# Kernel optimization log

Hardware: AMD Instinct MI355X
Metric: run time of the kernel (lower is better)

Reference implementation:

```python
import jax, jax.numpy as jnp
import numpy as np

B, N, K, NUM_CLASSES = 8, 4096, 20, 40


def _knn_idx(x, k):
    # x: [B, N, D] -> indices of k nearest neighbors (self excluded), [B, N, k]
    sq = jnp.sum(x * x, axis=-1)  # [B, N]
    dist = sq[:, :, None] + sq[:, None, :] - 2.0 * jnp.einsum('bnd,bmd->bnm', x, x)
    dist = jnp.where(jnp.eye(x.shape[1], dtype=bool)[None], jnp.inf, dist)
    return jax.lax.top_k(-dist, k)[1]


def _edge_conv(x, idx, params):
    # PyG EdgeConv with max aggregation: max_j MLP([x_i, x_j - x_i])
    x_j = jax.vmap(lambda xb, ib: xb[ib])(x, idx)              # [B, N, K, D]
    x_i = jnp.broadcast_to(x[:, :, None, :], x_j.shape)        # [B, N, K, D]
    h = jnp.concatenate([x_i, x_j - x_i], axis=-1)             # [B, N, K, 2D]
    for w, b in params:
        h = jax.nn.relu(h @ w + b)
    return jnp.max(h, axis=2)                                  # [B, N, out]


def setup_inputs() -> dict:
    key = jax.random.key(0)
    ks = jax.random.split(key, 12)

    def lin(k, i, o):  # torch Linear default init
        k1, k2 = jax.random.split(k)
        s = 1.0 / np.sqrt(i)
        return (jax.random.uniform(k1, (i, o), jnp.float32, -s, s),
                jax.random.uniform(k2, (o,), jnp.float32, -s, s))

    inp = {
        'pos': jax.random.normal(ks[0], (B * N, 3), jnp.float32),
        'batch': jnp.repeat(jnp.arange(B, dtype=jnp.int32), N),
    }
    names = [('m1w1', 'm1b1', 6, 64), ('m1w2', 'm1b2', 64, 64), ('m1w3', 'm1b3', 64, 64),
             ('m2w1', 'm2b1', 128, 128), ('m2w2', 'm2b2', 128, 128), ('m2w3', 'm2b3', 128, 256),
             ('lin0_w', 'lin0_b', 256, 512), ('lin1_w', 'lin1_b', 512, 256),
             ('lin2_w', 'lin2_b', 256, 256), ('lin3_w', 'lin3_b', 256, NUM_CLASSES)]
    for t, (wn, bn, i, o) in enumerate(names):
        w, b = lin(ks[t + 1], i, o)
        inp[wn] = w
        inp[bn] = b
    return inp


def reference(pos, batch, m1w1, m1b1, m1w2, m1b2, m1w3, m1b3,
              m2w1, m2b1, m2w2, m2b2, m2w3, m2b3,
              lin0_w, lin0_b, lin1_w, lin1_b, lin2_w, lin2_b, lin3_w, lin3_b):
    x = pos.reshape(B, N, 3)
    x = _edge_conv(x, _knn_idx(x, K), [(m1w1, m1b1), (m1w2, m1b2), (m1w3, m1b3)])   # [B,N,64]
    x = _edge_conv(x, _knn_idx(x, K), [(m2w1, m2b1), (m2w2, m2b2), (m2w3, m2b3)])   # [B,N,256]
    x = jax.nn.relu(x @ lin0_w + lin0_b)                                            # [B,N,512]
    x = jax.ops.segment_max(x.reshape(B * N, -1), batch, num_segments=B)            # [B,512]
    x = jax.nn.relu(x @ lin1_w + lin1_b)
    x = jax.nn.relu(x @ lin2_w + lin2_b)   # dropout is identity in eval mode
    x = x @ lin3_w + lin3_b
    return jax.nn.log_softmax(x, axis=-1)
```

## Files before the change

### kernel.cpp

```cpp
#include <hip/hip_runtime.h>

#define DEVI static __device__ __forceinline__

typedef __attribute__((ext_vector_type(4))) float f32x4;
typedef __attribute__((ext_vector_type(8))) short short8;
typedef __attribute__((ext_vector_type(4))) short short4v;
typedef __attribute__((ext_vector_type(8))) __bf16 bf16x8;

#define N_    4096
#define KNN_  20
#define NPTS  32768

DEVI unsigned short f2bf(float f){
  unsigned u = __float_as_uint(f);
  u += 0x7FFFu + ((u >> 16) & 1u);
  return (unsigned short)(u >> 16);
}
DEVI float bf2f(unsigned short s){ return __uint_as_float(((unsigned)s) << 16); }
DEVI float bf2fs(short s){ return __uint_as_float(((unsigned)(unsigned short)s) << 16); }
DEVI unsigned umin32(unsigned a, unsigned b){ return a < b ? a : b; }
DEVI unsigned umax32(unsigned a, unsigned b){ return a > b ? a : b; }

DEVI f32x4 mfma16(short8 a, short8 b, f32x4 c){
  return __builtin_amdgcn_mfma_f32_16x16x32_bf16(
      __builtin_bit_cast(bf16x8, a), __builtin_bit_cast(bf16x8, b), c, 0, 0, 0);
}

DEVI short8 lds_frag(const unsigned short* buf, int row, int k0, int strideS, int swzMask){
  return *(const short8*)(buf + row*strideS + (k0 ^ ((row & swzMask) << 3)));
}
DEVI void lds_put8(unsigned short* buf, int row, int k0, int strideS, int swzMask, short8 v){
  *(short8*)(buf + row*strideS + (k0 ^ ((row & swzMask) << 3))) = v;
}

DEVI void ins32(unsigned K, unsigned (&a)[20]){
#pragma unroll
  for (int t = 19; t >= 1; --t) a[t] = umin32(a[t], umax32(a[t-1], K));
  a[0] = umin32(a[0], K);
}
DEVI void ins64(double K, double (&a)[20]){
#pragma unroll
  for (int t = 19; t >= 1; --t) a[t] = fmin(a[t], fmax(a[t-1], K));
  a[0] = fmin(a[0], K);
}

DEVI void stage_body(const float* __restrict__ src, unsigned short* __restrict__ dh,
                     unsigned short* __restrict__ dl, int K, int Nw, int KT, int lblk){
  int tid = lblk*256 + (int)threadIdx.x;
  int l = tid & 63;
  int kk = (tid >> 6) % KT;
  int nt = tid / (64*KT);
  int n = nt*16 + (l & 15);
  int kb = kk*32 + ((l >> 4) << 3);
#pragma unroll
  for (int e=0;e<8;++e){
    int k = kb + e;
    float w = (k < K) ? src[(size_t)k*Nw + n] : 0.f;
    unsigned short h = f2bf(w);
    dh[(size_t)tid*8 + e] = h;
    if (dl) dl[(size_t)tid*8 + e] = f2bf(w - bf2f(h));
  }
}

__global__ __launch_bounds__(256) void stage_all_k(const float* __restrict__ pos,
    unsigned short* __restrict__ p3h, unsigned short* __restrict__ p3l, float* __restrict__ nrm3,
    const float* __restrict__ m1w1, const float* __restrict__ m1w2, const float* __restrict__ m1w3,
    const float* __restrict__ m2w1, const float* __restrict__ m2w2, const float* __restrict__ m2w3,
    const float* __restrict__ l0w,
    unsigned short* __restrict__ W1h, unsigned short* __restrict__ W1l,
    unsigned short* __restrict__ W2h, unsigned short* __restrict__ W2l,
    unsigned short* __restrict__ W3h, unsigned short* __restrict__ W3l,
    unsigned short* __restrict__ V1, unsigned short* __restrict__ V2, unsigned short* __restrict__ V3,
    unsigned short* __restrict__ W0){
  const int blk = blockIdx.x;
  if (blk < 128){
    int p = blk*256 + (int)threadIdx.x;
    float x = pos[(size_t)p*3], y = pos[(size_t)p*3+1], z = pos[(size_t)p*3+2];
    float v[8] = {x, y, z, 0.f, 0.f, 0.f, 0.f, 0.f};
#pragma unroll
    for (int c = 0; c < 8; ++c){
      unsigned short h = f2bf(v[c]);
      p3h[(size_t)p*8 + c] = h;
      p3l[(size_t)p*8 + c] = f2bf(v[c] - bf2f(h));
    }
    nrm3[p] = fmaf(x, x, fmaf(y, y, z*z));
    return;
  }
  int b = blk - 128;
  if      (b < 1)  stage_body(m1w1, W1h, W1l, 6,   64,  1, b);
  else if (b < 3)  stage_body(m1w2, W2h, W2l, 64,  64,  2, b-1);
  else if (b < 5)  stage_body(m1w3, W3h, W3l, 64,  64,  2, b-3);
  else if (b < 13) stage_body(m2w1, V1, nullptr, 128, 128, 4, b-5);
  else if (b < 21) stage_body(m2w2, V2, nullptr, 128, 128, 4, b-13);
  else if (b < 37) stage_body(m2w3, V3, nullptr, 128, 256, 4, b-21);
  else             stage_body(l0w,  W0, nullptr, 256, 512, 8, b-37);
}

template<int MODE>
__global__ __launch_bounds__(256) void knn_k(const unsigned short* __restrict__ Xh,
                                             const unsigned short* __restrict__ Xl,
                                             const float* __restrict__ nrm,
                                             unsigned* __restrict__ pk){
  constexpr int BSTR = MODE ? 4096 : 512;
  constexpr int OBL  = MODE ? 16384 : 2048;
  constexpr int OBUF = MODE ? 32768 : 4096;
  constexpr int OTHR = OBUF + 6144;
  constexpr int OSQ  = OTHR + 256;
  constexpr int SM   = MODE ? (OSQ + 512) : 15360;
  __shared__ __align__(16) char smem[SM];
  unsigned short* BhA = (unsigned short*)(smem);
  unsigned short* BlA = (unsigned short*)(smem + OBL);
  unsigned* buf      = (unsigned*)(smem + OBUF);
  unsigned* rowThr   = (unsigned*)(smem + OTHR);
  float* sqjA        = (float*)(smem + OSQ);
  unsigned* mD       = (unsigned*)(smem);

  const int blk = blockIdx.x;
  const int rt = blk & 63, ch = (blk >> 6) & 1, bb = blk >> 7;
  const int rowbase = rt * 64, cbase = ch * 2048;
  const size_t gb = (size_t)bb * N_;
  const int tid = threadIdx.x, lane = tid & 63, wid = tid >> 6;
  const int l15 = lane & 15, g = lane >> 4, kL = g << 3, r0 = g << 2;
  const int qidx = wid*16 + l15;

  if (tid < 64) rowThr[tid] = 0xFFFFFFFFu;

  short8 qh0 = {0,0,0,0,0,0,0,0}, qh1 = {0,0,0,0,0,0,0,0};
  short8 ql0 = {0,0,0,0,0,0,0,0}, ql1 = {0,0,0,0,0,0,0,0};
  if (MODE == 1){
    const size_t ab = (gb + rowbase + qidx) * 64;
    qh0 = *(const short8*)(Xh + ab + kL);
    qh1 = *(const short8*)(Xh + ab + 32 + kL);
    ql0 = *(const short8*)(Xl + ab + kL);
    ql1 = *(const short8*)(Xl + ab + 32 + kL);
  } else {
    if (g == 0){
      const size_t ab = (gb + rowbase + qidx) * 8;
      qh0 = *(const short8*)(Xh + ab);
      ql0 = *(const short8*)(Xl + ab);
    }
  }
  const float si = nrm[gb + rowbase + qidx];

  unsigned arr[20];
#pragma unroll
  for (int t = 0; t < 20; ++t) arr[t] = 0xFFFFFFFFu;
  int cnt = 0;
  bool selfR[4];
#pragma unroll
  for (int r = 0; r < 4; ++r) selfR[r] = (l15 == r0 + r);

  if (MODE == 1){
    for (int f = tid; f < 512; f += 256){
      int lf = f & 63, half = (f >> 6) & 1, ct = f >> 7;
      int row = ct*16 + (lf & 15);
      int col = half*32 + ((lf >> 4) << 3);
      const size_t src = (gb + cbase + row) * 64 + col;
      *(short8*)(BhA + f*8) = *(const short8*)(Xh + src);
      *(short8*)(BlA + f*8) = *(const short8*)(Xl + src);
    }
  } else {
    if (tid < 64)       *(short8*)(BhA + tid*8)      = *(const short8*)(Xh + (gb + cbase + tid)*8);
    else if (tid < 128) *(short8*)(BlA + (tid-64)*8) = *(const short8*)(Xl + (gb + cbase + (tid-64))*8);
  }
  if (tid < 64) sqjA[tid] = nrm[gb + cbase + tid];
  __syncthreads();

  for (int c = 0; c < 32; ++c){
    const int cur = c & 1;
    const unsigned short* Bh = BhA + cur*BSTR;
    const unsigned short* Bl = BlA + cur*BSTR;
    const float* sqj = sqjA + cur*64;
    const bool selfTile = (cbase + c*64 == rowbase);
    const bool more = (c + 1 < 32);

    short8 nh0 = {0,0,0,0,0,0,0,0}, nh1 = {0,0,0,0,0,0,0,0};
    short8 nl0 = {0,0,0,0,0,0,0,0}, nl1 = {0,0,0,0,0,0,0,0};
    float nsq = 0.f;
    if (more){
      if (MODE == 1){
#pragma unroll
        for (int ff = 0; ff < 2; ++ff){
          int f = tid + ff*256;
          int lf = f & 63, half = (f >> 6) & 1, ct = f >> 7;
          int row = ct*16 + (lf & 15);
          int col = half*32 + ((lf >> 4) << 3);
          const size_t src = (gb + cbase + (c+1)*64 + row) * 64 + col;
          if (ff == 0){ nh0 = *(const short8*)(Xh + src); nl0 = *(const short8*)(Xl + src); }
          else        { nh1 = *(const short8*)(Xh + src); nl1 = *(const short8*)(Xl + src); }
        }
      } else {
        if (tid < 64)       nh0 = *(const short8*)(Xh + (gb + cbase + (c+1)*64 + tid)*8);
        else if (tid < 128) nl0 = *(const short8*)(Xl + (gb + cbase + (c+1)*64 + (tid-64))*8);
      }
      if (tid < 64) nsq = nrm[gb + cbase + (c+1)*64 + tid];
    }

    unsigned kb16[16];
#pragma unroll
    for (int ct = 0; ct < 4; ++ct){
      f32x4 acc = {0.f,0.f,0.f,0.f};
      if (MODE == 1){
        const int fb = lane*8;
        short8 ch0 = *(const short8*)(Bh + (ct*2+0)*512 + fb);
        short8 ch1 = *(const short8*)(Bh + (ct*2+1)*512 + fb);
        short8 cl0 = *(const short8*)(Bl + (ct*2+0)*512 + fb);
        short8 cl1 = *(const short8*)(Bl + (ct*2+1)*512 + fb);
        acc = mfma16(ch0, qh0, acc); acc = mfma16(ch1, qh1, acc);
        acc = mfma16(cl0, qh0, acc); acc = mfma16(cl1, qh1, acc);
        acc = mfma16(ch0, ql0, acc); acc = mfma16(ch1, ql1, acc);
      } else {
        short8 cb = {0,0,0,0,0,0,0,0}, cl_ = {0,0,0,0,0,0,0,0};
        if (g == 0){
          cb  = *(const short8*)(Bh + (ct*16 + l15)*8);
          cl_ = *(const short8*)(Bl + (ct*16 + l15)*8);
        }
        acc = mfma16(cb,  qh0, acc);
        acc = mfma16(cl_, qh0, acc);
        acc = mfma16(cb,  ql0, acc);
      }
      f32x4 sj4 = *(const f32x4*)(sqj + ct*16 + r0);
#pragma unroll
      for (int r = 0; r < 4; ++r){
        float dv = fmaxf(fmaf(-2.f, acc[r], si + sj4[r]), 0.f);
        kb16[ct*4 + r] = __float_as_uint(dv);
      }
    }

    {
      unsigned thrUp = rowThr[qidx] | 0x7FFu;
#pragma unroll
      for (int i = 0; i < 16; ++i){
        unsigned b = kb16[i];
        if (b <= thrUp){
          if (selfTile && (i >> 2) == wid && selfR[i & 3]) continue;
          unsigned kb = (b & ~0x7FFu) | (unsigned)(c*64 + (i >> 2)*16 + r0 + (i & 3));
          if (cnt < 6){ buf[cnt*256 + tid] = kb; ++cnt; }
          else ins32(kb, arr);
        }
      }
      for (int t = 0; t < cnt; ++t) ins32(buf[t*256 + tid], arr);
      cnt = 0;
      atomicMin(&rowThr[qidx], arr[19]);
    }

    if (more){
      unsigned short* BhN = BhA + (cur^1)*BSTR;
      unsigned short* BlN = BlA + (cur^1)*BSTR;
      if (MODE == 1){
        *(short8*)(BhN + tid*8)       = nh0;
        *(short8*)(BhN + (tid+256)*8) = nh1;
        *(short8*)(BlN + tid*8)       = nl0;
        *(short8*)(BlN + (tid+256)*8) = nl1;
      } else {
        if (tid < 64)       *(short8*)(BhN + tid*8)      = nh0;
        else if (tid < 128) *(short8*)(BlN + (tid-64)*8) = nl0;
      }
      if (tid < 64) sqjA[(cur^1)*64 + tid] = nsq;
    }
    __syncthreads();
  }
  __syncthreads();
  if (g > 0){
#pragma unroll
    for (int t = 0; t < 20; ++t) mD[(qidx*3 + g-1)*20 + t] = arr[t];
  }
  __syncthreads();
  if (g == 0){
    for (int gg = 0; gg < 3; ++gg)
#pragma unroll
      for (int t = 0; t < 20; ++t) ins32(mD[(qidx*3 + gg)*20 + t], arr);
    const size_t gp = gb + rowbase + qidx;
#pragma unroll
    for (int t = 0; t < 20; ++t) pk[((size_t)(ch*20 + t))*NPTS + gp] = arr[t];
  }
}

__global__ __launch_bounds__(256) void knn_merge_k(const unsigned* __restrict__ pk,
                                                   int* __restrict__ idx){
  const int p = blockIdx.x*256 + threadIdx.x;
  double arr[20];
#pragma unroll
  for (int t = 0; t < 20; ++t){
    unsigned k = pk[(size_t)t*NPTS + p];
    unsigned long long K = (((unsigned long long)(k & ~0x7FFu)) << 1) | (k & 0x7FFu);
    arr[t] = __builtin_bit_cast(double, K);
  }
#pragma unroll
  for (int t = 0; t < 20; ++t){
    unsigned k = pk[(size_t)(20 + t)*NPTS + p];
    unsigned long long K = (((unsigned long long)(k & ~0x7FFu)) << 1) | (2048u + (k & 0x7FFu));
    ins64(__builtin_bit_cast(double, K), arr);
  }
  int* o = idx + (size_t)p*KNN_;
#pragma unroll
  for (int t = 0; t < 20; ++t)
    o[t] = (int)(__builtin_bit_cast(unsigned long long, arr[t]) & 0xFFFu);
}

__global__ __launch_bounds__(256) void ec1_k(const float* __restrict__ pos, const int* __restrict__ idx1,
    const unsigned short* __restrict__ W1h, const unsigned short* __restrict__ W1l,
    const unsigned short* __restrict__ W2h, const unsigned short* __restrict__ W2l,
    const unsigned short* __restrict__ W3h, const unsigned short* __restrict__ W3l,
    const float* __restrict__ b1, const float* __restrict__ b2, const float* __restrict__ b3,
    unsigned short* __restrict__ x1h, unsigned short* __restrict__ x1l, float* __restrict__ nrm1){
  __shared__ __align__(16) char smem[51200];
  unsigned short* Ah  = (unsigned short*)(smem);
  unsigned short* Al  = (unsigned short*)(smem + 5120);
  unsigned short* H1h = (unsigned short*)(smem + 10240);
  unsigned short* H1l = (unsigned short*)(smem + 20480);
  unsigned short* H2h = (unsigned short*)(smem + 30720);
  unsigned short* H2l = (unsigned short*)(smem + 40960);
  float* dump = (float*)(smem);
  const int p0 = blockIdx.x * 4;
  const int bb = p0 >> 12;
  const int tid = threadIdx.x, lane = tid & 63, wid = tid >> 6;
  const int l15 = lane & 15, g = lane >> 4, r0 = g << 2;

  if (tid < 80){
    int p = p0 + tid/20, slot = tid%20;
    int j = idx1[(size_t)p*KNN_ + slot];
    int gj = (bb << 12) + j;
    float a6[6];
    a6[0] = pos[(size_t)p*3]; a6[1] = pos[(size_t)p*3+1]; a6[2] = pos[(size_t)p*3+2];
    a6[3] = pos[(size_t)gj*3]   - a6[0];
    a6[4] = pos[(size_t)gj*3+1] - a6[1];
    a6[5] = pos[(size_t)gj*3+2] - a6[2];
    int mt = tid >> 4, lrow = tid & 15;
    short8 vh, vl, zz = {0,0,0,0,0,0,0,0};
#pragma unroll
    for (int c=0;c<8;++c){
      float v = (c < 6) ? a6[c] : 0.f;
      unsigned short h = f2bf(v);
      vh[c] = (short)h;
      vl[c] = (short)f2bf(v - bf2f(h));
    }
    *(short8*)(Ah + (mt*64 + lrow)*8) = vh;
    *(short8*)(Al + (mt*64 + lrow)*8) = vl;
#pragma unroll
    for (int gg=1;gg<4;++gg){
      *(short8*)(Ah + (mt*64 + gg*16 + lrow)*8) = zz;
      *(short8*)(Al + (mt*64 + gg*16 + lrow)*8) = zz;
    }
  }
  __syncthreads();
  const int nt = wid;
  const int kk2 = nt >> 1, sub2 = (nt & 1)*2 + (g >> 1), e0 = (g & 1)*4;
  {
    short8 wh = *(const short8*)(W1h + ((size_t)nt*64 + lane)*8);
    short8 wl = *(const short8*)(W1l + ((size_t)nt*64 + lane)*8);
    f32x4 b4 = *(const f32x4*)(b1 + nt*16 + r0);
    for (int mt=0; mt<5; ++mt){
      short8 ah = *(const short8*)(Ah + (mt*64 + lane)*8);
      short8 al = *(const short8*)(Al + (mt*64 + lane)*8);
      f32x4 acc = {0.f,0.f,0.f,0.f};
      acc = mfma16(wh, ah, acc);
      acc = mfma16(wl, ah, acc);
      acc = mfma16(wh, al, acc);
      short4v vh4, vl4;
#pragma unroll
      for (int r=0;r<4;++r){
        float v = fmaxf(acc[r] + b4[r], 0.f);
        unsigned short h = f2bf(v);
        vh4[r] = (short)h;
        vl4[r] = (short)f2bf(v - bf2f(h));
      }
      *(short4v*)(H1h + ((mt*2 + kk2)*64 + sub2*16 + l15)*8 + e0) = vh4;
      *(short4v*)(H1l + ((mt*2 + kk2)*64 + sub2*16 + l15)*8 + e0) = vl4;
    }
  }
  __syncthreads();
  {
    short8 wh0 = *(const short8*)(W2h + ((size_t)(nt*2+0)*64 + lane)*8);
    short8 wh1 = *(const short8*)(W2h + ((size_t)(nt*2+1)*64 + lane)*8);
    short8 wl0 = *(const short8*)(W2l + ((size_t)(nt*2+0)*64 + lane)*8);
    short8 wl1 = *(const short8*)(W2l + ((size_t)(nt*2+1)*64 + lane)*8);
    f32x4 b4 = *(const f32x4*)(b2 + nt*16 + r0);
    for (int mt=0; mt<5; ++mt){
      short8 ah0 = *(const short8*)(H1h + ((mt*2+0)*64 + lane)*8);
      short8 ah1 = *(const short8*)(H1h + ((mt*2+1)*64 + lane)*8);
      short8 al0 = *(const short8*)(H1l + ((mt*2+0)*64 + lane)*8);
      short8 al1 = *(const short8*)(H1l + ((mt*2+1)*64 + lane)*8);
      f32x4 acc = {0.f,0.f,0.f,0.f};
      acc = mfma16(wh0, ah0, acc); acc = mfma16(wh1, ah1, acc);
      acc = mfma16(wl0, ah0, acc); acc = mfma16(wl1, ah1, acc);
      acc = mfma16(wh0, al0, acc); acc = mfma16(wh1, al1, acc);
      short4v vh4, vl4;
#pragma unroll
      for (int r=0;r<4;++r){
        float v = fmaxf(acc[r] + b4[r], 0.f);
        unsigned short h = f2bf(v);
        vh4[r] = (short)h;
        vl4[r] = (short)f2bf(v - bf2f(h));
      }
      *(short4v*)(H2h + ((mt*2 + kk2)*64 + sub2*16 + l15)*8 + e0) = vh4;
      *(short4v*)(H2l + ((mt*2 + kk2)*64 + sub2*16 + l15)*8 + e0) = vl4;
    }
  }
  __syncthreads();
  {
    short8 wh0 = *(const short8*)(W3h + ((size_t)(nt*2+0)*64 + lane)*8);
    short8 wh1 = *(const short8*)(W3h + ((size_t)(nt*2+1)*64 + lane)*8);
    short8 wl0 = *(const short8*)(W3l + ((size_t)(nt*2+0)*64 + lane)*8);
    short8 wl1 = *(const short8*)(W3l + ((size_t)(nt*2+1)*64 + lane)*8);
    f32x4 b4 = *(const f32x4*)(b3 + nt*16 + r0);
    for (int mt=0; mt<5; ++mt){
      short8 ah0 = *(const short8*)(H2h + ((mt*2+0)*64 + lane)*8);
      short8 ah1 = *(const short8*)(H2h + ((mt*2+1)*64 + lane)*8);
      short8 al0 = *(const short8*)(H2l + ((mt*2+0)*64 + lane)*8);
      short8 al1 = *(const short8*)(H2l + ((mt*2+1)*64 + lane)*8);
      f32x4 acc = {0.f,0.f,0.f,0.f};
      acc = mfma16(wh0, ah0, acc); acc = mfma16(wh1, ah1, acc);
      acc = mfma16(wl0, ah0, acc); acc = mfma16(wl1, ah1, acc);
      acc = mfma16(wh0, al0, acc); acc = mfma16(wh1, al1, acc);
      f32x4 o;
#pragma unroll
      for (int r=0;r<4;++r) o[r] = fmaxf(acc[r] + b4[r], 0.f);
      int edge = mt*16 + l15;
      *(f32x4*)(dump + edge*68 + nt*16 + r0) = o;
    }
  }
  __syncthreads();
  if (tid < 64){
    int p = tid >> 4, c4 = tid & 15;
    int st = tid % 20;
    float mx[4] = {0.f,0.f,0.f,0.f};
    for (int e=0;e<20;++e){
      int ee = st + e; if (ee >= 20) ee -= 20;
      f32x4 v = *(const f32x4*)(dump + (p*20 + ee)*68 + c4*4);
#pragma unroll
      for (int r=0;r<4;++r) mx[r] = fmaxf(mx[r], v[r]);
    }
    int gp = p0 + p;
    short4v h4, l4;
    float s = 0.f;
#pragma unroll
    for (int r=0;r<4;++r){
      float m = mx[r];
      unsigned short h = f2bf(m);
      h4[r] = (short)h;
      l4[r] = (short)f2bf(m - bf2f(h));
      s = fmaf(m, m, s);
    }
    *(short4v*)(x1h + (size_t)gp*64 + c4*4) = h4;
    *(short4v*)(x1l + (size_t)gp*64 + c4*4) = l4;
    s += __shfl_xor(s, 1); s += __shfl_xor(s, 2); s += __shfl_xor(s, 4); s += __shfl_xor(s, 8);
    if (c4 == 0) nrm1[gp] = s;
  }
}

__global__ __launch_bounds__(256) void ec2_k(const unsigned short* __restrict__ x1h, const int* __restrict__ idx2,
    const unsigned short* __restrict__ V1, const unsigned short* __restrict__ V2, const unsigned short* __restrict__ V3,
    const float* __restrict__ b1, const float* __restrict__ b2, const float* __restrict__ b3,
    unsigned short* __restrict__ x2b){
  __shared__ __align__(16) char smem[81920];
  unsigned short* A  = (unsigned short*)(smem);
  unsigned short* H1 = (unsigned short*)(smem + 40960);
  const int p0 = blockIdx.x * 8, bb = p0 >> 12;
  const int tid = threadIdx.x, lane = tid & 63, wid = tid >> 6;
  const int l15 = lane & 15, r0 = (lane >> 4) << 2;

  if (tid < 160){
    int p = p0 + tid/20, slot = tid%20;
    int j = idx2[(size_t)p*KNN_ + slot];
    int gj = (bb << 12) + j;
    const unsigned short* xi = x1h + (size_t)p*64;
    const unsigned short* xj = x1h + (size_t)gj*64;
    int mt = tid >> 4, lrow = tid & 15;
#pragma unroll
    for (int q=0;q<8;++q){
      short8 vi = *(const short8*)(xi + q*8);
      short8 vj = *(const short8*)(xj + q*8);
      short8 vd;
#pragma unroll
      for (int c=0;c<8;++c) vd[c] = (short)f2bf(bf2fs(vj[c]) - bf2fs(vi[c]));
      *(short8*)(A + (((mt*4 + (q>>2))*64) + (q&3)*16 + lrow)*8) = vi;
      *(short8*)(A + (((mt*4 + 2 + (q>>2))*64) + (q&3)*16 + lrow)*8) = vd;
    }
  }
  __syncthreads();

  {
    short8 w[2][4];
#pragma unroll
    for (int ni=0;ni<2;++ni)
#pragma unroll
      for (int kk=0;kk<4;++kk)
        w[ni][kk] = *(const short8*)(V1 + ((size_t)((wid*2+ni)*4+kk)*64 + lane)*8);
    f32x4 b4[2];
    b4[0] = *(const f32x4*)(b1 + (wid*2+0)*16 + r0);
    b4[1] = *(const f32x4*)(b1 + (wid*2+1)*16 + r0);
    for (int mt=0; mt<10; ++mt){
      short8 bfr[4];
#pragma unroll
      for (int kk=0;kk<4;++kk) bfr[kk] = *(const short8*)(A + ((mt*4+kk)*64 + lane)*8);
#pragma unroll
      for (int ni=0;ni<2;++ni){
        int nt = wid*2 + ni;
        f32x4 acc = {0.f,0.f,0.f,0.f};
#pragma unroll
        for (int kk=0;kk<4;++kk) acc = mfma16(w[ni][kk], bfr[kk], acc);
        short4v v4;
#pragma unroll
        for (int r=0;r<4;++r) v4[r] = (short)f2bf(fmaxf(acc[r] + b4[ni][r], 0.f));
        int kk2 = nt >> 1, sub2 = (nt & 1)*2 + (r0 >> 3);
        *(short4v*)(H1 + ((mt*4+kk2)*64 + sub2*16 + l15)*8 + (r0 & 4)) = v4;
      }
    }
  }
  __syncthreads();
  {
    short8 w[2][4];
#pragma unroll
    for (int ni=0;ni<2;++ni)
#pragma unroll
      for (int kk=0;kk<4;++kk)
        w[ni][kk] = *(const short8*)(V2 + ((size_t)((wid*2+ni)*4+kk)*64 + lane)*8);
    f32x4 b4[2];
    b4[0] = *(const f32x4*)(b2 + (wid*2+0)*16 + r0);
    b4[1] = *(const f32x4*)(b2 + (wid*2+1)*16 + r0);
    for (int mt=0; mt<10; ++mt){
      short8 bfr[4];
#pragma unroll
      for (int kk=0;kk<4;++kk) bfr[kk] = *(const short8*)(H1 + ((mt*4+kk)*64 + lane)*8);
#pragma unroll
      for (int ni=0;ni<2;++ni){
        int nt = wid*2 + ni;
        f32x4 acc = {0.f,0.f,0.f,0.f};
#pragma unroll
        for (int kk=0;kk<4;++kk) acc = mfma16(w[ni][kk], bfr[kk], acc);
        short4v v4;
#pragma unroll
        for (int r=0;r<4;++r) v4[r] = (short)f2bf(fmaxf(acc[r] + b4[ni][r], 0.f));
        int kk2 = nt >> 1, sub2 = (nt & 1)*2 + (r0 >> 3);
        *(short4v*)(A + ((mt*4+kk2)*64 + sub2*16 + l15)*8 + (r0 & 4)) = v4;
      }
    }
  }
  __syncthreads();
  for (int g2=0; g2<2; ++g2){
    {
      short8 w[2][4];
#pragma unroll
      for (int ni=0;ni<2;++ni)
#pragma unroll
        for (int kk=0;kk<4;++kk)
          w[ni][kk] = *(const short8*)(V3 + ((size_t)((g2*8 + wid*2+ni)*4+kk)*64 + lane)*8);
      f32x4 b4[2];
      b4[0] = *(const f32x4*)(b3 + (g2*8 + wid*2+0)*16 + r0);
      b4[1] = *(const f32x4*)(b3 + (g2*8 + wid*2+1)*16 + r0);
      for (int mt=0; mt<10; ++mt){
        short8 bfr[4];
#pragma unroll
        for (int kk=0;kk<4;++kk) bfr[kk] = *(const short8*)(A + ((mt*4+kk)*64 + lane)*8);
#pragma unroll
        for (int ni=0;ni<2;++ni){
          int ntl = wid*2 + ni;
          f32x4 acc = {0.f,0.f,0.f,0.f};
#pragma unroll
          for (int kk=0;kk<4;++kk) acc = mfma16(w[ni][kk], bfr[kk], acc);
          short4v v4;
#pragma unroll
          for (int r=0;r<4;++r) v4[r] = (short)f2bf(fmaxf(acc[r] + b4[ni][r], 0.f));
          int kk2 = ntl >> 1, sub2 = (ntl & 1)*2 + (r0 >> 3);
          *(short4v*)(H1 + ((mt*4+kk2)*64 + sub2*16 + l15)*8 + (r0 & 4)) = v4;
        }
      }
    }
    __syncthreads();
    if (tid < 128){
      int p = tid >> 4, c8 = tid & 15;
      int kk = c8 >> 2, sub = c8 & 3;
      unsigned short mx[8];
#pragma unroll
      for (int e=0;e<8;++e) mx[e] = 0;
      for (int e=0;e<20;++e){
        int ee = e + p + c8; ee -= (ee >= 20) ? 20 : 0; ee -= (ee >= 20) ? 20 : 0;
        int row = p*20 + ee;
        short8 v = *(const short8*)(H1 + (((row>>4)*4 + kk)*64 + sub*16 + (row & 15))*8);
#pragma unroll
        for (int k2=0;k2<8;++k2){
          unsigned short u = (unsigned short)v[k2];
          mx[k2] = u > mx[k2] ? u : mx[k2];
        }
      }
      short8 o;
#pragma unroll
      for (int k2=0;k2<8;++k2) o[k2] = (short)mx[k2];
      *(short8*)(x2b + (size_t)(p0 + p)*256 + g2*128 + c8*8) = o;
    }
    __syncthreads();
  }
}

__global__ __launch_bounds__(256) void lin0_k(const unsigned short* __restrict__ x2b, const unsigned short* __restrict__ W0s,
                                              const float* __restrict__ b0, unsigned* __restrict__ pool){
  __shared__ __align__(16) char smem[67584];
  unsigned short* A = (unsigned short*)(smem);
  unsigned* ploc = (unsigned*)(smem + 65536);
  const int blk = blockIdx.x; const size_t row0 = (size_t)blk * 128; const int bb = blk >> 5;
  const int tid = threadIdx.x, lane = tid & 63, wid = tid >> 6;
  for (int it = tid; it < 4096; it += 256){
    int row = it >> 5, q = (it & 31) << 3;
    lds_put8(A, row, q, 256, 7, *(const short8*)(x2b + (row0 + row)*256 + q));
  }
  ploc[tid] = 0u; ploc[tid+256] = 0u;
  __syncthreads();
  const int l15 = lane & 15, kL = (lane >> 4) << 3;
  short8 af[2][8];
#pragma unroll
  for (int m=0;m<2;++m)
#pragma unroll
    for (int kk=0;kk<8;++kk)
      af[m][kk] = lds_frag(A, (wid*2+m)*16 + l15, kk*32 + kL, 256, 7);
  for (int nt=0; nt<32; ++nt){
    f32x4 a0 = {0.f,0.f,0.f,0.f}, a1 = {0.f,0.f,0.f,0.f};
#pragma unroll
    for (int kk=0;kk<8;++kk){
      short8 w = *(const short8*)(W0s + ((size_t)(nt*8+kk)*64 + lane)*8);
      a0 = mfma16(af[0][kk], w, a0);
      a1 = mfma16(af[1][kk], w, a1);
    }
    int col = nt*16 + l15;
    float m = fmaxf(fmaxf(fmaxf(a0[0],a0[1]),fmaxf(a0[2],a0[3])),
                    fmaxf(fmaxf(a1[0],a1[1]),fmaxf(a1[2],a1[3])));
    m = fmaxf(m + b0[col], 0.f);
    atomicMax(&ploc[col], __float_as_uint(m));
  }
  __syncthreads();
  atomicMax(&pool[(size_t)bb*512 + tid], ploc[tid]);
  atomicMax(&pool[(size_t)bb*512 + tid + 256], ploc[tid+256]);
}

__global__ __launch_bounds__(256) void head8_k(const unsigned* __restrict__ pool,
    const float* __restrict__ w1, const float* __restrict__ bb1,
    const float* __restrict__ w2, const float* __restrict__ bb2,
    const float* __restrict__ w3, const float* __restrict__ bb3,
    float* __restrict__ out){
  __shared__ float pl[512];
  __shared__ float y1[256];
  __shared__ float y2[256];
  __shared__ float lg[40];
  const int row = blockIdx.x;
  const int tid = threadIdx.x;
  for (int it = tid; it < 512; it += 256) pl[it] = __uint_as_float(pool[row*512 + it]);
  __syncthreads();
  {
    float acc = bb1[tid];
    for (int k=0;k<512;++k) acc = fmaf(pl[k], w1[(size_t)k*256 + tid], acc);
    y1[tid] = fmaxf(acc, 0.f);
  }
  __syncthreads();
  {
    float acc = bb2[tid];
    for (int k=0;k<256;++k) acc = fmaf(y1[k], w2[(size_t)k*256 + tid], acc);
    y2[tid] = fmaxf(acc, 0.f);
  }
  __syncthreads();
  if (tid < 40){
    float acc = bb3[tid];
    for (int k=0;k<256;++k) acc = fmaf(y2[k], w3[(size_t)k*40 + tid], acc);
    lg[tid] = acc;
  }
  __syncthreads();
  if (tid < 40){
    float m = -__builtin_inff();
    for (int c2=0;c2<40;++c2) m = fmaxf(m, lg[c2]);
    float s = 0.f;
    for (int c2=0;c2<40;++c2) s += expf(lg[c2] - m);
    out[row*40 + tid] = lg[tid] - m - logf(s);
  }
}

extern "C" void kernel_launch(void* const* d_in, const int* in_sizes, int n_in,
                              void* d_out, int out_size, void* d_ws, size_t ws_size,
                              hipStream_t stream){
  (void)in_sizes; (void)n_in; (void)out_size; (void)ws_size;
  const float* pos  = (const float*)d_in[0];
  const float* m1w1 = (const float*)d_in[2];  const float* m1b1 = (const float*)d_in[3];
  const float* m1w2 = (const float*)d_in[4];  const float* m1b2 = (const float*)d_in[5];
  const float* m1w3 = (const float*)d_in[6];  const float* m1b3 = (const float*)d_in[7];
  const float* m2w1 = (const float*)d_in[8];  const float* m2b1 = (const float*)d_in[9];
  const float* m2w2 = (const float*)d_in[10]; const float* m2b2 = (const float*)d_in[11];
  const float* m2w3 = (const float*)d_in[12]; const float* m2b3 = (const float*)d_in[13];
  const float* l0w  = (const float*)d_in[14]; const float* l0b  = (const float*)d_in[15];
  const float* l1w  = (const float*)d_in[16]; const float* l1b  = (const float*)d_in[17];
  const float* l2w  = (const float*)d_in[18]; const float* l2b  = (const float*)d_in[19];
  const float* l3w  = (const float*)d_in[20]; const float* l3b  = (const float*)d_in[21];

  char* ws = (char*)d_ws;
  size_t o = 0;
  auto alloc = [&](size_t bytes){ size_t r = o; o += (bytes + 255) & ~(size_t)255; return r; };
  size_t o_idx1 = alloc((size_t)NPTS*20*4);
  size_t o_idx2 = alloc((size_t)NPTS*20*4);
  size_t o_x1h  = alloc((size_t)NPTS*64*2);
  size_t o_x1l  = alloc((size_t)NPTS*64*2);
  size_t o_nrm  = alloc((size_t)NPTS*4);
  size_t o_x2b  = alloc((size_t)NPTS*256*2);
  size_t o_pool = alloc(8*512*4);
  size_t o_p3h  = alloc((size_t)NPTS*8*2);
  size_t o_p3l  = alloc((size_t)NPTS*8*2);
  size_t o_nrm3 = alloc((size_t)NPTS*4);
  size_t o_pk   = alloc((size_t)2*20*NPTS*4);
  size_t o_W1h = alloc(4*1*64*8*2),  o_W1l = alloc(4*1*64*8*2);
  size_t o_W2h = alloc(4*2*64*8*2),  o_W2l = alloc(4*2*64*8*2);
  size_t o_W3h = alloc(4*2*64*8*2),  o_W3l = alloc(4*2*64*8*2);
  size_t o_V1  = alloc(8*4*64*8*2);
  size_t o_V2  = alloc(8*4*64*8*2);
  size_t o_V3  = alloc(16*4*64*8*2);
  size_t o_W0  = alloc(32*8*64*8*2);

  hipMemsetAsync(ws + o_pool, 0, 8*512*4, stream);

  stage_all_k<<<229,256,0,stream>>>(pos,
      (unsigned short*)(ws+o_p3h), (unsigned short*)(ws+o_p3l), (float*)(ws+o_nrm3),
      m1w1, m1w2, m1w3, m2w1, m2w2, m2w3, l0w,
      (unsigned short*)(ws+o_W1h), (unsigned short*)(ws+o_W1l),
      (unsigned short*)(ws+o_W2h), (unsigned short*)(ws+o_W2l),
      (unsigned short*)(ws+o_W3h), (unsigned short*)(ws+o_W3l),
      (unsigned short*)(ws+o_V1), (unsigned short*)(ws+o_V2), (unsigned short*)(ws+o_V3),
      (unsigned short*)(ws+o_W0));

  knn_k<0><<<1024,256,0,stream>>>((const unsigned short*)(ws+o_p3h), (const unsigned short*)(ws+o_p3l),
                                  (const float*)(ws+o_nrm3), (unsigned*)(ws+o_pk));
  knn_merge_k<<<128,256,0,stream>>>((const unsigned*)(ws+o_pk), (int*)(ws+o_idx1));

  ec1_k<<<8192,256,0,stream>>>(pos, (const int*)(ws+o_idx1),
      (const unsigned short*)(ws+o_W1h), (const unsigned short*)(ws+o_W1l),
      (const unsigned short*)(ws+o_W2h), (const unsigned short*)(ws+o_W2l),
      (const unsigned short*)(ws+o_W3h), (const unsigned short*)(ws+o_W3l),
      m1b1, m1b2, m1b3,
      (unsigned short*)(ws+o_x1h), (unsigned short*)(ws+o_x1l), (float*)(ws+o_nrm));

  knn_k<1><<<1024,256,0,stream>>>((const unsigned short*)(ws+o_x1h), (const unsigned short*)(ws+o_x1l),
                                  (const float*)(ws+o_nrm), (unsigned*)(ws+o_pk));
  knn_merge_k<<<128,256,0,stream>>>((const unsigned*)(ws+o_pk), (int*)(ws+o_idx2));

  ec2_k<<<4096,256,0,stream>>>((const unsigned short*)(ws+o_x1h), (const int*)(ws+o_idx2),
      (const unsigned short*)(ws+o_V1), (const unsigned short*)(ws+o_V2), (const unsigned short*)(ws+o_V3),
      m2b1, m2b2, m2b3, (unsigned short*)(ws+o_x2b));

  lin0_k<<<256,256,0,stream>>>((const unsigned short*)(ws+o_x2b), (const unsigned short*)(ws+o_W0),
                               l0b, (unsigned*)(ws+o_pool));

  head8_k<<<8,256,0,stream>>>((const unsigned*)(ws+o_pool), l1w, l1b, l2w, l2b, l3w, l3b, (float*)d_out);
}
```

Before: 575.8 us.

## Enlarge kNN blocks to 128 query rows with 512 threads sharing candidate tiles

The kNN kernel now runs 512 threads per block covering 128 query rows instead of 64, so each staged candidate tile in shared memory serves twice as many queries. This halves the global loads of candidate tiles, and each thread now loads one short8 per tile instead of two. Self-exclusion moves out of the inner selection loop into a single masked write before the loop. The cost is larger shared memory per block, half as many blocks, and possibly lower occupancy or load balance.

```diff
diff --git a/kernel.cpp b/kernel.cpp
--- a/kernel.cpp
+++ b/kernel.cpp
@@ -97,16 +97,16 @@
 }
 
 template<int MODE>
-__global__ __launch_bounds__(256) void knn_k(const unsigned short* __restrict__ Xh,
+__global__ __launch_bounds__(512) void knn_k(const unsigned short* __restrict__ Xh,
                                              const unsigned short* __restrict__ Xl,
                                              const float* __restrict__ nrm,
                                              unsigned* __restrict__ pk){
   constexpr int BSTR = MODE ? 4096 : 512;
   constexpr int OBL  = MODE ? 16384 : 2048;
   constexpr int OBUF = MODE ? 32768 : 4096;
-  constexpr int OTHR = OBUF + 6144;
-  constexpr int OSQ  = OTHR + 256;
-  constexpr int SM   = MODE ? (OSQ + 512) : 15360;
+  constexpr int OTHR = OBUF + 12288;
+  constexpr int OSQ  = OTHR + 512;
+  constexpr int SM   = MODE ? (OSQ + 512) : 30720;
   __shared__ __align__(16) char smem[SM];
   unsigned short* BhA = (unsigned short*)(smem);
   unsigned short* BlA = (unsigned short*)(smem + OBL);
@@ -116,14 +116,14 @@
   unsigned* mD       = (unsigned*)(smem);
 
   const int blk = blockIdx.x;
-  const int rt = blk & 63, ch = (blk >> 6) & 1, bb = blk >> 7;
-  const int rowbase = rt * 64, cbase = ch * 2048;
+  const int rt = blk & 31, ch = (blk >> 5) & 1, bb = blk >> 6;
+  const int rowbase = rt * 128, cbase = ch * 2048;
   const size_t gb = (size_t)bb * N_;
   const int tid = threadIdx.x, lane = tid & 63, wid = tid >> 6;
   const int l15 = lane & 15, g = lane >> 4, kL = g << 3, r0 = g << 2;
   const int qidx = wid*16 + l15;
 
-  if (tid < 64) rowThr[tid] = 0xFFFFFFFFu;
+  if (tid < 128) rowThr[tid] = 0xFFFFFFFFu;
 
   short8 qh0 = {0,0,0,0,0,0,0,0}, qh1 = {0,0,0,0,0,0,0,0};
   short8 ql0 = {0,0,0,0,0,0,0,0}, ql1 = {0,0,0,0,0,0,0,0};
@@ -146,19 +146,18 @@
 #pragma unroll
   for (int t = 0; t < 20; ++t) arr[t] = 0xFFFFFFFFu;
   int cnt = 0;
-  bool selfR[4];
-#pragma unroll
-  for (int r = 0; r < 4; ++r) selfR[r] = (l15 == r0 + r);
+  const int selfTileBase = rowbase + (qidx & 64);
+  const int sl = qidx & 63;
+  const bool selfMine = (((sl >> 2) & 3) == g);
+  const int selfSlot = ((sl >> 4) << 2) + (sl & 3);
 
   if (MODE == 1){
-    for (int f = tid; f < 512; f += 256){
-      int lf = f & 63, half = (f >> 6) & 1, ct = f >> 7;
-      int row = ct*16 + (lf & 15);
-      int col = half*32 + ((lf >> 4) << 3);
-      const size_t src = (gb + cbase + row) * 64 + col;
-      *(short8*)(BhA + f*8) = *(const short8*)(Xh + src);
-      *(short8*)(BlA + f*8) = *(const short8*)(Xl + src);
-    }
+    int lf = tid & 63, half = (tid >> 6) & 1, ct = tid >> 7;
+    int row = ct*16 + (lf & 15);
+    int col = half*32 + ((lf >> 4) << 3);
+    const size_t src = (gb + cbase + row) * 64 + col;
+    *(short8*)(BhA + tid*8) = *(const short8*)(Xh + src);
+    *(short8*)(BlA + tid*8) = *(const short8*)(Xl + src);
   } else {
     if (tid < 64)       *(short8*)(BhA + tid*8)      = *(const short8*)(Xh + (gb + cbase + tid)*8);
     else if (tid < 128) *(short8*)(BlA + (tid-64)*8) = *(const short8*)(Xl + (gb + cbase + (tid-64))*8);
@@ -171,24 +170,18 @@
     const unsigned short* Bh = BhA + cur*BSTR;
     const unsigned short* Bl = BlA + cur*BSTR;
     const float* sqj = sqjA + cur*64;
-    const bool selfTile = (cbase + c*64 == rowbase);
     const bool more = (c + 1 < 32);
 
-    short8 nh0 = {0,0,0,0,0,0,0,0}, nh1 = {0,0,0,0,0,0,0,0};
-    short8 nl0 = {0,0,0,0,0,0,0,0}, nl1 = {0,0,0,0,0,0,0,0};
+    short8 nh0 = {0,0,0,0,0,0,0,0}, nl0 = {0,0,0,0,0,0,0,0};
     float nsq = 0.f;
     if (more){
       if (MODE == 1){
-#pragma unroll
-        for (int ff = 0; ff < 2; ++ff){
-          int f = tid + ff*256;
-          int lf = f & 63, half = (f >> 6) & 1, ct = f >> 7;
-          int row = ct*16 + (lf & 15);
-          int col = half*32 + ((lf >> 4) << 3);
-          const size_t src = (gb + cbase + (c+1)*64 + row) * 64 + col;
-          if (ff == 0){ nh0 = *(const short8*)(Xh + src); nl0 = *(const short8*)(Xl + src); }
-          else        { nh1 = *(const short8*)(Xh + src); nl1 = *(const short8*)(Xl + src); }
-        }
+        int lf = tid & 63, half = (tid >> 6) & 1, ct = tid >> 7;
+        int row = ct*16 + (lf & 15);
+        int col = half*32 + ((lf >> 4) << 3);
+        const size_t src = (gb + cbase + (c+1)*64 + row) * 64 + col;
+        nh0 = *(const short8*)(Xh + src);
+        nl0 = *(const short8*)(Xl + src);
       } else {
         if (tid < 64)       nh0 = *(const short8*)(Xh + (gb + cbase + (c+1)*64 + tid)*8);
         else if (tid < 128) nl0 = *(const short8*)(Xl + (gb + cbase + (c+1)*64 + (tid-64))*8);
@@ -226,20 +219,21 @@
         kb16[ct*4 + r] = __float_as_uint(dv);
       }
     }
+    if (selfMine && (cbase + c*64 == selfTileBase)) kb16[selfSlot] = 0xFFFFFFFFu;
 
     {
       unsigned thrUp = rowThr[qidx] | 0x7FFu;
+      unsigned cidb = (unsigned)(c*64 + r0);
 #pragma unroll
       for (int i = 0; i < 16; ++i){
         unsigned b = kb16[i];
         if (b <= thrUp){
-          if (selfTile && (i >> 2) == wid && selfR[i & 3]) continue;
-          unsigned kb = (b & ~0x7FFu) | (unsigned)(c*64 + (i >> 2)*16 + r0 + (i & 3));
-          if (cnt < 6){ buf[cnt*256 + tid] = kb; ++cnt; }
+          unsigned kb = (b & ~0x7FFu) | (cidb + (((i >> 2) << 4) + (i & 3)));
+          if (cnt < 6){ buf[cnt*512 + tid] = kb; ++cnt; }
           else ins32(kb, arr);
         }
       }
-      for (int t = 0; t < cnt; ++t) ins32(buf[t*256 + tid], arr);
+      for (int t = 0; t < cnt; ++t) ins32(buf[t*512 + tid], arr);
       cnt = 0;
       atomicMin(&rowThr[qidx], arr[19]);
     }
@@ -248,10 +242,8 @@
       unsigned short* BhN = BhA + (cur^1)*BSTR;
       unsigned short* BlN = BlA + (cur^1)*BSTR;
       if (MODE == 1){
-        *(short8*)(BhN + tid*8)       = nh0;
-        *(short8*)(BhN + (tid+256)*8) = nh1;
-        *(short8*)(BlN + tid*8)       = nl0;
-        *(short8*)(BlN + (tid+256)*8) = nl1;
+        *(short8*)(BhN + tid*8) = nh0;
+        *(short8*)(BlN + tid*8) = nl0;
       } else {
         if (tid < 64)       *(short8*)(BhN + tid*8)      = nh0;
         else if (tid < 128) *(short8*)(BlN + (tid-64)*8) = nl0;
@@ -721,8 +713,8 @@
       (unsigned short*)(ws+o_V1), (unsigned short*)(ws+o_V2), (unsigned short*)(ws+o_V3),
       (unsigned short*)(ws+o_W0));
 
-  knn_k<0><<<1024,256,0,stream>>>((const unsigned short*)(ws+o_p3h), (const unsigned short*)(ws+o_p3l),
-                                  (const float*)(ws+o_nrm3), (unsigned*)(ws+o_pk));
+  knn_k<0><<<512,512,0,stream>>>((const unsigned short*)(ws+o_p3h), (const unsigned short*)(ws+o_p3l),
+                                 (const float*)(ws+o_nrm3), (unsigned*)(ws+o_pk));
   knn_merge_k<<<128,256,0,stream>>>((const unsigned*)(ws+o_pk), (int*)(ws+o_idx1));
 
   ec1_k<<<8192,256,0,stream>>>(pos, (const int*)(ws+o_idx1),
@@ -732,8 +724,8 @@
       m1b1, m1b2, m1b3,
       (unsigned short*)(ws+o_x1h), (unsigned short*)(ws+o_x1l), (float*)(ws+o_nrm));
 
-  knn_k<1><<<1024,256,0,stream>>>((const unsigned short*)(ws+o_x1h), (const unsigned short*)(ws+o_x1l),
-                                  (const float*)(ws+o_nrm), (unsigned*)(ws+o_pk));
+  knn_k<1><<<512,512,0,stream>>>((const unsigned short*)(ws+o_x1h), (const unsigned short*)(ws+o_x1l),
+                                 (const float*)(ws+o_nrm), (unsigned*)(ws+o_pk));
   knn_merge_k<<<128,256,0,stream>>>((const unsigned*)(ws+o_pk), (int*)(ws+o_idx2));
 
   ec2_k<<<4096,256,0,stream>>>((const unsigned short*)(ws+o_x1h), (const int*)(ws+o_idx2),
```

New measurement: 580.7 us, median of 2. Within noise of the previous version (+0.8%).
